# Kernel optimization log

Hardware: AMD Instinct MI355X
Metric: run time of the kernel (lower is better)

## Reference

```python
import jax, jax.numpy as jnp
import numpy as np

N_NODES = 20000
N_EDGES = 120000
IN_CH = 128
HID = 128
OUT_CH = 40
N_LAYERS = 2


def _build_two_hop(edge_index_np, num_nodes):
    # Faithful to build_two_hop_edges: for each node i, set of neighbors-of-neighbors, minus i.
    row, col = edge_index_np[0], edge_index_np[1]
    deg = np.bincount(row, minlength=num_nodes)
    order = np.argsort(row, kind='stable')
    col_sorted = col[order]
    indptr = np.zeros(num_nodes + 1, dtype=np.int64)
    indptr[1:] = np.cumsum(deg)
    reps = deg[col]                      # second-hop fanout per edge
    starts = indptr[col]
    total = int(reps.sum())
    cum = np.cumsum(reps) - reps
    offs = np.arange(total, dtype=np.int64) - np.repeat(cum, reps)
    flat = np.repeat(starts, reps) + offs
    r2 = np.repeat(row, reps)
    c2 = col_sorted[flat]
    mask = r2 != c2                      # remove i from its own 2-hop set
    keys = r2[mask].astype(np.int64) * num_nodes + c2[mask].astype(np.int64)
    uk = np.unique(keys)                 # set-dedup semantics
    return np.stack([uk // num_nodes, uk % num_nodes], axis=0)


def setup_inputs() -> dict:
    key = jax.random.key(0)
    ks = jax.random.split(key, 10)
    x = jax.random.normal(ks[0], (N_NODES, IN_CH), dtype=jnp.float32)
    x0 = jax.random.normal(ks[1], (N_NODES, IN_CH), dtype=jnp.float32)
    edge_index = jax.random.randint(ks[2], (2, N_EDGES), 0, N_NODES, dtype=jnp.int64)
    ei_np = np.asarray(edge_index)
    edge_index_2hop = jnp.asarray(_build_two_hop(ei_np, N_NODES), dtype=jnp.int64)
    s_in = 1.0 / np.sqrt(IN_CH)
    s_h = 1.0 / np.sqrt(HID)
    in_W = jax.random.normal(ks[3], (IN_CH, HID), dtype=jnp.float32) * s_in
    skip_W = jax.random.normal(ks[4], (HID, HID), dtype=jnp.float32) * s_h
    conv_W = jax.random.normal(ks[5], (N_LAYERS, HID, HID), dtype=jnp.float32) * s_h
    conv_b = jax.random.normal(ks[6], (N_LAYERS, HID), dtype=jnp.float32) * 0.01
    fc_W = jax.random.normal(ks[7], (HID, OUT_CH), dtype=jnp.float32) * s_h
    fc_b = jax.random.normal(ks[8], (OUT_CH,), dtype=jnp.float32) * 0.01
    return {"x": x, "x0": x0, "edge_index": edge_index, "edge_index_2hop": edge_index_2hop,
            "in_W": in_W, "skip_W": skip_W, "conv_W": conv_W, "conv_b": conv_b,
            "fc_W": fc_W, "fc_b": fc_b}


def _gamma(x_agg, row, col, inv_deg, n):
    # gather -> squared diff -> per-node mean -> tanh ; p=2 so abs()**2 == square
    d = x_agg[row] - x_agg[col]                 # [E, H]
    s = jnp.sum(d * d, axis=-1)                 # [E]
    g = jax.ops.segment_sum(s, row, num_segments=n) * inv_deg
    return jnp.tanh(g)[:, None]                 # [N, 1], broadcasts over H


def _forward(x, x0, edge_index, edge_index_2hop, in_W, skip_W, conv_W, conv_b, fc_W, fc_b):
    n = x.shape[0]
    row, col = edge_index[0], edge_index[1]
    row2, col2 = edge_index_2hop[0], edge_index_2hop[1]
    h = x @ in_W
    h0 = x0 @ in_W
    x_skip = h0 @ skip_W                        # same every layer (skip_fc(x0))
    ones1 = jnp.ones(row.shape[0], dtype=h.dtype)
    ones2 = jnp.ones(row2.shape[0], dtype=h.dtype)
    inv_deg1 = 1.0 / (jax.ops.segment_sum(ones1, row, num_segments=n) + 1e-10)
    inv_deg2 = 1.0 / (jax.ops.segment_sum(ones2, row2, num_segments=n) + 1e-10)
    for l in range(conv_W.shape[0]):
        # GCNConv with normalize=None(False): plain sum-aggregation of transformed source feats
        m = h @ conv_W[l]
        x_agg = jax.nn.relu(jax.ops.segment_sum(m[row], col, num_segments=n) + conv_b[l])
        g_smooth = _gamma(x_agg, row, col, inv_deg1, n)
        g_squash = _gamma(x_agg, row2, col2, inv_deg2, n)
        denom = 1.0 + g_smooth + g_squash
        h = (h + g_smooth * x_agg + g_squash * x_skip) / denom
    return h @ fc_W + fc_b


def reference(x, x0, edge_index, edge_index_2hop, in_W, skip_W, conv_W, conv_b, fc_W, fc_b):
    return _forward(x, x0, edge_index, edge_index_2hop, in_W, skip_W, conv_W, conv_b, fc_W, fc_b)
```

## Files before the change

kernel.cpp:

```cpp
#include <hip/hip_runtime.h>
#include <hip/hip_bf16.h>

#define HIDC 128
#define OUTC 40
#define ASTR 136
#define PACKN (4 * 16384 + 6144)

typedef __hip_bfloat16 bf16;
typedef unsigned int uint32;
typedef __attribute__((ext_vector_type(8))) short s8v;
typedef __attribute__((ext_vector_type(4))) float f4v;

__device__ __forceinline__ unsigned short f2b(float v) {
    return __bfloat16_as_ushort(__float2bfloat16(v));
}
__device__ __forceinline__ int ldi(const int* p, size_t i, int is64) {
    return is64 ? p[2 * i] : p[i];
}
__device__ __forceinline__ float diff2(uint32 ua, uint32 ub) {
    float ax = __uint_as_float(ua << 16);
    float ay = __uint_as_float(ua & 0xFFFF0000u);
    float bx = __uint_as_float(ub << 16);
    float by = __uint_as_float(ub & 0xFFFF0000u);
    float d0 = ax - bx, d1 = ay - by;
    return d0 * d0 + d1 * d1;
}
__device__ __forceinline__ float dq4(uint4 a, uint4 b) {
    return diff2(a.x, b.x) + diff2(a.y, b.y) + diff2(a.z, b.z) + diff2(a.w, b.w);
}

__device__ __forceinline__ void mfma16(const unsigned short* a_lds, const unsigned short* Wp,
                                       int w, int lane, f4v acc[2]) {
    const int m = lane & 15;
    const int kq = (lane >> 4) * 8;
#pragma unroll
    for (int nt2 = 0; nt2 < 2; ++nt2) {
        const int nt = w * 2 + nt2;
        f4v a = {0.f, 0.f, 0.f, 0.f};
#pragma unroll
        for (int s = 0; s < 4; ++s) {
            s8v af = *(const s8v*)(a_lds + m * ASTR + s * 32 + kq);
            s8v bfv = *(const s8v*)(Wp + (((nt * 4 + s) * 64 + lane) * 8));
            a = __builtin_amdgcn_mfma_f32_16x16x32_bf16(af, bfv, a, 0, 0, 0);
        }
        acc[nt2] = a;
    }
}

__global__ void detect_zero(const uint32* __restrict__ x, const uint32* __restrict__ e1,
                            int* __restrict__ flags, int* __restrict__ cnt2, int n2) {
    for (int i = blockIdx.x * 256 + threadIdx.x; i < n2; i += gridDim.x * 256) cnt2[i] = 0;
    if (blockIdx.x != 0) return;
    __shared__ int sh[2];
    const int t = threadIdx.x;
    if (t < 2) sh[t] = 0;
    __syncthreads();
    int cnt = 0;
    for (int i = t; i < 1024; i += 256) {
        uint32 w = x[i] & 0xFFFFu;
        uint32 e = (w >> 7) & 0xFFu;
        if ((e >= 100u && e <= 140u) || (w & 0x7FFFu) == 0u) cnt++;
    }
    int zc = (e1[2 * t + 1] == 0) ? 1 : 0;
    atomicAdd(&sh[0], cnt);
    atomicAdd(&sh[1], zc);
    __syncthreads();
    if (t == 0) {
        flags[0] = (sh[0] >= 512) ? 1 : 0;
        flags[1] = (sh[1] >= 255) ? 1 : 0;
        flags[2] = 1;
    }
}

__global__ void pack_k(const float* __restrict__ inW, const float* __restrict__ skW,
                       const float* __restrict__ cW, const float* __restrict__ fW,
                       unsigned short* __restrict__ Wp) {
    int idx = blockIdx.x * 256 + threadIdx.x;
    if (idx >= PACKN) return;
    if (idx < 4 * 16384) {
        int mat = idx >> 14, r = idx & 16383;
        const float* W = (mat == 0) ? inW
                       : (mat == 1) ? skW
                                    : cW + (size_t)(mat - 2) * HIDC * HIDC;
        int j = r & 7, lane = (r >> 3) & 63, s = (r >> 9) & 3, nt = r >> 11;
        int k = s * 32 + (lane >> 4) * 8 + j;
        int ncol = nt * 16 + (lane & 15);
        Wp[idx] = f2b(W[k * HIDC + ncol]);
    } else {
        int r = idx - 4 * 16384;
        int j = r & 7, lane = (r >> 3) & 63, s = (r >> 9) & 3, nt = r >> 11;
        int k = s * 32 + (lane >> 4) * 8 + j;
        int ncol = nt * 16 + (lane & 15);
        Wp[idx] = (ncol < OUTC) ? f2b(fW[k * OUTC + ncol]) : 0;
    }
}

__global__ void prep_k(const int* __restrict__ e2, int E2, int* __restrict__ indptr2,
                       const int* __restrict__ e1, int E1, int* __restrict__ cntC,
                       int* __restrict__ cntR, int* __restrict__ flags, int n, int L) {
    const int is64 = flags[1];
    for (int i = blockIdx.x * 256 + threadIdx.x; i < L; i += gridDim.x * 256) {
        if (i < E2 - 1 && ldi(e2, i, is64) > ldi(e2, i + 1, is64)) flags[2] = 0;
        if (i <= n) {
            int lo = 0, hi = E2;
            while (lo < hi) {
                int mid = (lo + hi) >> 1;
                if (ldi(e2, mid, is64) < i) lo = mid + 1; else hi = mid;
            }
            indptr2[i] = lo;
        }
        if (i < E1) {
            atomicAdd(&cntC[ldi(e1, (size_t)E1 + i, is64)], 1);
            atomicAdd(&cntR[ldi(e1, i, is64)], 1);
        }
    }
}

__global__ void beacon_k(const int* __restrict__ flags, float wsterm, float* __restrict__ out) {
    if (threadIdx.x == 0)
        out[0] = 100.f + 1600.f * flags[0] + 800.f * flags[1] + wsterm;
}

__global__ void scanA2(const int* __restrict__ cntC, const int* __restrict__ cntR,
                       int* __restrict__ indptrC, int* __restrict__ indptrR,
                       int* __restrict__ totals, int n, int nb) {
    __shared__ int smem[1024];
    const int half = (blockIdx.x >= nb) ? 1 : 0;
    const int b = blockIdx.x - half * nb;
    const int* cnt = half ? cntR : cntC;
    int* indptr = half ? indptrR : indptrC;
    const int tid = threadIdx.x;
    const int i = b * 1024 + tid;
    int v = (i < n) ? cnt[i] : 0;
    smem[tid] = v;
    __syncthreads();
    for (int off = 1; off < 1024; off <<= 1) {
        int tv = (tid >= off) ? smem[tid - off] : 0;
        __syncthreads();
        smem[tid] += tv;
        __syncthreads();
    }
    if (i < n) indptr[i] = smem[tid] - v;
    if (tid == 1023) totals[blockIdx.x] = smem[1023];
}

__global__ void scanB2(int* __restrict__ indptrC, int* __restrict__ indptrR,
                       int* __restrict__ curC, int* __restrict__ curR,
                       const int* __restrict__ totals, int n, int nb) {
    const int half = (blockIdx.x >= nb) ? 1 : 0;
    const int b = blockIdx.x - half * nb;
    int* indptr = half ? indptrR : indptrC;
    int* cursor = half ? curR : curC;
    const int* tot = totals + half * nb;
    const int i = b * 1024 + threadIdx.x;
    int off = 0;
    for (int k = 0; k < b; ++k) off += tot[k];
    if (i < n) {
        int fin = indptr[i] + off;
        indptr[i] = fin;
        cursor[i] = fin;
    }
    if (b == nb - 1 && threadIdx.x == 1023) indptr[n] = off + tot[b];
}

__global__ void fill_both(const int* __restrict__ e, int E, int* __restrict__ curC,
                          int* __restrict__ curR, int* __restrict__ permA,
                          int* __restrict__ permG, const int* __restrict__ flags) {
    const int is64 = flags[1];
    int i = blockIdx.x * 256 + threadIdx.x;
    if (i >= E) return;
    int r = ldi(e, i, is64);
    int c = ldi(e, (size_t)E + i, is64);
    permA[atomicAdd(&curC[c], 1)] = r;
    permG[atomicAdd(&curR[r], 1)] = c;
}

__global__ void zero_id2_fb(float* __restrict__ id2, int n, const int* __restrict__ flags) {
    if (flags[2] != 0) return;
    for (int i = blockIdx.x * 256 + threadIdx.x; i < n; i += gridDim.x * 256) id2[i] = 0.f;
}
__global__ void deg_count_fb(const int* __restrict__ e, int E, float* __restrict__ deg,
                             const int* __restrict__ flags) {
    if (flags[2] != 0) return;
    const int is64 = flags[1];
    for (int i = blockIdx.x * 256 + threadIdx.x; i < E; i += gridDim.x * 256)
        atomicAdd(&deg[ldi(e, i, is64)], 1.0f);
}
__global__ void invert_fb(float* __restrict__ d, int n, const int* __restrict__ flags) {
    if (flags[2] != 0) return;
    for (int i = blockIdx.x * 256 + threadIdx.x; i < n; i += gridDim.x * 256)
        d[i] = 1.0f / (d[i] + 1e-10f);
}
__global__ void gamma_edge_fb(const uint32* __restrict__ aggbf, const int* __restrict__ e, int E,
                              float* __restrict__ g, const int* __restrict__ flags) {
    if (flags[2] != 0) return;
    const int is64 = flags[1];
    const int lane = threadIdx.x & 63;
    const int l16 = lane & 15, sub = lane >> 4;
    const int wv0 = (blockIdx.x * 256 + threadIdx.x) >> 6;
    const int totalW = (gridDim.x * 256) >> 6;
    for (size_t base = (size_t)wv0 * 4; base < (size_t)E; base += (size_t)totalW * 4) {
        size_t ed = base + sub;
        float s = 0.f;
        int r = 0;
        bool act = ed < (size_t)E;
        if (act) {
            r = is64 ? e[2 * ed] : e[ed];
            int c = is64 ? e[2 * ((size_t)E + ed)] : e[(size_t)E + ed];
            uint4 a = ((const uint4*)(aggbf + (size_t)r * 64))[l16];
            uint4 b = ((const uint4*)(aggbf + (size_t)c * 64))[l16];
            s = dq4(a, b);
        }
#pragma unroll
        for (int off = 1; off <= 8; off <<= 1) s += __shfl_xor(s, off);
        if (l16 == 0 && act) atomicAdd(&g[r], s);
    }
}
__global__ void update_fb(float* __restrict__ h, const unsigned short* __restrict__ aggbf,
                          const float* __restrict__ xskip, const float* __restrict__ g1,
                          const float* __restrict__ g2, const int* __restrict__ indptrR,
                          const float* __restrict__ id2, unsigned short* __restrict__ hbf,
                          const int* __restrict__ flags, int n) {
    if (flags[2] != 0) return;
    for (int idx = blockIdx.x * 256 + threadIdx.x; idx < n * 32; idx += gridDim.x * 256) {
        int node = idx >> 5;
        float d1 = (float)(indptrR[node + 1] - indptrR[node]);
        float gs = tanhf(g1[node] / (d1 + 1e-10f));
        float gq = tanhf(g2[node] * id2[node]);
        float inv = 1.0f / (1.0f + gs + gq);
        float4 hv = ((const float4*)h)[idx];
        uint2 ub = ((const uint2*)aggbf)[idx];
        float4 av;
        av.x = __uint_as_float(ub.x << 16);
        av.y = __uint_as_float(ub.x & 0xFFFF0000u);
        av.z = __uint_as_float(ub.y << 16);
        av.w = __uint_as_float(ub.y & 0xFFFF0000u);
        float4 sv = ((const float4*)xskip)[idx];
        hv.x = (hv.x + gs * av.x + gq * sv.x) * inv;
        hv.y = (hv.y + gs * av.y + gq * sv.y) * inv;
        hv.z = (hv.z + gs * av.z + gq * sv.z) * inv;
        hv.w = (hv.w + gs * av.w + gq * sv.w) * inv;
        ((float4*)h)[idx] = hv;
        uint2 hb;
        hb.x = ((uint32)f2b(hv.y) << 16) | f2b(hv.x);
        hb.y = ((uint32)f2b(hv.w) << 16) | f2b(hv.z);
        ((uint2*)hbf)[idx] = hb;
    }
}

__global__ void gemm_head(const float* __restrict__ x, const float* __restrict__ x0,
                          const unsigned short* __restrict__ inWp,
                          const unsigned short* __restrict__ skWp,
                          float* __restrict__ h, unsigned short* __restrict__ hbf,
                          float* __restrict__ xskip, int n, int gB) {
    __shared__ unsigned short a_bf[16 * ASTR];
    const int pathB = (blockIdx.x >= gB) ? 1 : 0;
    const int row0 = (blockIdx.x - pathB * gB) * 16;
    const int t = threadIdx.x;
    const int lane = t & 63, w = t >> 6;
    {
        const float* A = pathB ? x0 : x;
        int i = t >> 4;
        int c0 = (t & 15) * 8;
        int r = row0 + i;
        unsigned short u[8];
        if (r < n) {
            const float* p = A + (size_t)r * HIDC + c0;
            float4 v0 = ((const float4*)p)[0];
            float4 v1 = ((const float4*)p)[1];
            u[0] = f2b(v0.x); u[1] = f2b(v0.y); u[2] = f2b(v0.z); u[3] = f2b(v0.w);
            u[4] = f2b(v1.x); u[5] = f2b(v1.y); u[6] = f2b(v1.z); u[7] = f2b(v1.w);
        } else {
#pragma unroll
            for (int j2 = 0; j2 < 8; ++j2) u[j2] = 0;
        }
        *(s8v*)(a_bf + i * ASTR + c0) = *(s8v*)u;
    }
    __syncthreads();
    f4v acc[2];
    mfma16(a_bf, inWp, w, lane, acc);
    if (!pathB) {
#pragma unroll
        for (int nt2 = 0; nt2 < 2; ++nt2) {
            int col = (w * 2 + nt2) * 16 + (lane & 15);
            int rb = row0 + (lane >> 4) * 4;
#pragma unroll
            for (int q = 0; q < 4; ++q)
                if (rb + q < n) {
                    h[(size_t)(rb + q) * HIDC + col] = acc[nt2][q];
                    hbf[(size_t)(rb + q) * HIDC + col] = f2b(acc[nt2][q]);
                }
        }
        return;
    }
    __syncthreads();
#pragma unroll
    for (int nt2 = 0; nt2 < 2; ++nt2) {
        int col = (w * 2 + nt2) * 16 + (lane & 15);
        int rb = (lane >> 4) * 4;
#pragma unroll
        for (int q = 0; q < 4; ++q)
            a_bf[(rb + q) * ASTR + col] = f2b(acc[nt2][q]);
    }
    __syncthreads();
    mfma16(a_bf, skWp, w, lane, acc);
#pragma unroll
    for (int nt2 = 0; nt2 < 2; ++nt2) {
        int col = (w * 2 + nt2) * 16 + (lane & 15);
        int rb = row0 + (lane >> 4) * 4;
#pragma unroll
        for (int q = 0; q < 4; ++q)
            if (rb + q < n) xskip[(size_t)(rb + q) * HIDC + col] = acc[nt2][q];
    }
}

__global__ void agg_gemm_relu(const unsigned short* __restrict__ hbf,
                              const int* __restrict__ indptrC,
                              const int* __restrict__ permA,
                              const unsigned short* __restrict__ cWp,
                              const float* __restrict__ cbv,
                              unsigned short* __restrict__ aggbf,
                              float* __restrict__ g2, const int* __restrict__ flags, int n) {
    if (flags[2] == 0) {
        int i = blockIdx.x * 256 + threadIdx.x;
        if (i < n) g2[i] = 0.f;
    }
    __shared__ unsigned short a_bf[16 * ASTR];
    const int row0 = blockIdx.x * 16;
    const int lane = threadIdx.x & 63, w = threadIdx.x >> 6;
    {
        const int rb = row0 + w * 4;
        float2 acc[4];
        int js[4], je[4], nxt[4];
#pragma unroll
        for (int i = 0; i < 4; ++i) {
            acc[i] = make_float2(0.f, 0.f);
            int r = rb + i;
            js[i] = (r < n) ? indptrC[r] : 0;
            je[i] = (r < n) ? indptrC[r + 1] : 0;
            nxt[i] = (js[i] < je[i]) ? permA[js[i]] : 0;
        }
        int maxd = 0;
#pragma unroll
        for (int i = 0; i < 4; ++i) maxd = max(maxd, je[i] - js[i]);
        for (int jj = 0; jj < maxd; ++jj) {
#pragma unroll
            for (int i = 0; i < 4; ++i) {
                int j = js[i] + jj;
                if (j < je[i]) {
                    int src = nxt[i];
                    int j2 = j + 1;
                    nxt[i] = (j2 < je[i]) ? permA[j2] : 0;
                    uint32 v = ((const uint32*)(hbf + (size_t)src * HIDC))[lane];
                    acc[i].x += __uint_as_float(v << 16);
                    acc[i].y += __uint_as_float(v & 0xFFFF0000u);
                }
            }
        }
#pragma unroll
        for (int i = 0; i < 4; ++i) {
            unsigned short* p = a_bf + (w * 4 + i) * ASTR + 2 * lane;
            p[0] = f2b(acc[i].x);
            p[1] = f2b(acc[i].y);
        }
    }
    __syncthreads();
    f4v acc2[2];
    mfma16(a_bf, cWp, w, lane, acc2);
#pragma unroll
    for (int nt2 = 0; nt2 < 2; ++nt2) {
        int col = (w * 2 + nt2) * 16 + (lane & 15);
        float bias = cbv[col];
        int rb = row0 + (lane >> 4) * 4;
#pragma unroll
        for (int q = 0; q < 4; ++q) {
            int r = rb + q;
            if (r < n) aggbf[(size_t)r * HIDC + col] = f2b(fmaxf(acc2[nt2][q] + bias, 0.f));
        }
    }
}

__global__ void gamma_update(const uint32* __restrict__ aggbf, const int* __restrict__ indptrR,
                             const int* __restrict__ permG, const int* __restrict__ e2, int E2,
                             const int* __restrict__ indptr2, float* __restrict__ h,
                             const float* __restrict__ xskip, float* __restrict__ g1,
                             unsigned short* __restrict__ hbf,
                             const int* __restrict__ flags, int n) {
    int r = (blockIdx.x * 256 + threadIdx.x) >> 6;
    if (r >= n) return;
    const int lane = threadIdx.x & 63;
    const int l16 = lane & 15, sub = lane >> 4;
    const int sorted = flags[2];
    const int is64 = flags[1];
    const int js1 = indptrR[r], je1 = indptrR[r + 1];
    uint4 a = ((const uint4*)(aggbf + (size_t)r * 64))[l16];
    float s1 = 0.f;
    for (int j = js1 + sub; j < je1; j += 4) {
        int c = permG[j];
        uint4 b = ((const uint4*)(aggbf + (size_t)c * 64))[l16];
        s1 += dq4(a, b);
    }
#pragma unroll
    for (int off = 32; off; off >>= 1) s1 += __shfl_xor(s1, off);
    if (sorted == 0) {
        if (lane == 0) g1[r] = s1;
        return;
    }
    const int js2 = indptr2[r], je2 = indptr2[r + 1];
    float s2a = 0.f, s2b = 0.f, s2c = 0.f, s2d = 0.f;
    int j = js2 + sub;
    for (; j + 12 < je2; j += 16) {
        int c0 = is64 ? e2[2 * ((size_t)E2 + j)] : e2[(size_t)E2 + j];
        int c1 = is64 ? e2[2 * ((size_t)E2 + j + 4)] : e2[(size_t)E2 + j + 4];
        int c2 = is64 ? e2[2 * ((size_t)E2 + j + 8)] : e2[(size_t)E2 + j + 8];
        int c3 = is64 ? e2[2 * ((size_t)E2 + j + 12)] : e2[(size_t)E2 + j + 12];
        uint4 b0 = ((const uint4*)(aggbf + (size_t)c0 * 64))[l16];
        uint4 b1 = ((const uint4*)(aggbf + (size_t)c1 * 64))[l16];
        uint4 b2 = ((const uint4*)(aggbf + (size_t)c2 * 64))[l16];
        uint4 b3 = ((const uint4*)(aggbf + (size_t)c3 * 64))[l16];
        s2a += dq4(a, b0);
        s2b += dq4(a, b1);
        s2c += dq4(a, b2);
        s2d += dq4(a, b3);
    }
    for (; j < je2; j += 4) {
        int c = is64 ? e2[2 * ((size_t)E2 + j)] : e2[(size_t)E2 + j];
        uint4 b = ((const uint4*)(aggbf + (size_t)c * 64))[l16];
        s2a += dq4(a, b);
    }
    float s2 = (s2a + s2b) + (s2c + s2d);
#pragma unroll
    for (int off = 32; off; off >>= 1) s2 += __shfl_xor(s2, off);
    float gs = tanhf(s1 / ((float)(je1 - js1) + 1e-10f));
    float gq = tanhf(s2 / ((float)(je2 - js2) + 1e-10f));
    float inv = 1.0f / (1.0f + gs + gq);
    size_t base = (size_t)r * 64 + lane;
    float2 hv = ((float2*)h)[base];
    uint32 ub = aggbf[base];
    float avx = __uint_as_float(ub << 16);
    float avy = __uint_as_float(ub & 0xFFFF0000u);
    float2 sv = ((const float2*)xskip)[base];
    hv.x = (hv.x + gs * avx + gq * sv.x) * inv;
    hv.y = (hv.y + gs * avy + gq * sv.y) * inv;
    ((float2*)h)[base] = hv;
    ((uint32*)hbf)[base] = ((uint32)f2b(hv.y) << 16) | f2b(hv.x);
}

__global__ void gemm_out(const unsigned short* __restrict__ hbf,
                         const unsigned short* __restrict__ fWp,
                         const float* __restrict__ fcb, float* __restrict__ out, int n) {
    __shared__ unsigned short a_bf[16 * ASTR];
    const int row0 = blockIdx.x * 16;
    const int t = threadIdx.x;
    const int lane = t & 63, w = t >> 6;
    {
        int i = t >> 4;
        int c0 = (t & 15) * 8;
        int r = row0 + i;
        s8v v = {0, 0, 0, 0, 0, 0, 0, 0};
        if (r < n) v = *(const s8v*)(hbf + (size_t)r * HIDC + c0);
        *(s8v*)(a_bf + i * ASTR + c0) = v;
    }
    __syncthreads();
    if (w < 3) {
        const int m = lane & 15;
        const int kq = (lane >> 4) * 8;
        f4v a = {0.f, 0.f, 0.f, 0.f};
#pragma unroll
        for (int s = 0; s < 4; ++s) {
            s8v af = *(const s8v*)(a_bf + m * ASTR + s * 32 + kq);
            s8v bfv = *(const s8v*)(fWp + (((w * 4 + s) * 64 + lane) * 8));
            a = __builtin_amdgcn_mfma_f32_16x16x32_bf16(af, bfv, a, 0, 0, 0);
        }
        int col = w * 16 + (lane & 15);
        if (col < OUTC) {
            float bias = fcb[col];
            int rb = row0 + (lane >> 4) * 4;
#pragma unroll
            for (int q = 0; q < 4; ++q)
                if (rb + q < n) out[(size_t)(rb + q) * OUTC + col] = a[q] + bias;
        }
    }
}

extern "C" void kernel_launch(void* const* d_in, const int* in_sizes, int n_in,
                              void* d_out, int out_size, void* d_ws, size_t ws_size,
                              hipStream_t stream) {
    const float* x   = (const float*)d_in[0];
    const float* x0  = (const float*)d_in[1];
    const int*   e1  = (const int*)d_in[2];
    const int*   e2  = (const int*)d_in[3];
    const float* inW = (const float*)d_in[4];
    const float* skW = (const float*)d_in[5];
    const float* cW  = (const float*)d_in[6];
    const float* cb  = (const float*)d_in[7];
    const float* fW  = (const float*)d_in[8];
    const float* fb  = (const float*)d_in[9];
    float* out = (float*)d_out;

    const int N = in_sizes[0] / HIDC;
    int div = 2;
    if (in_sizes[2] / 2 != 120000 && in_sizes[2] / 4 == 120000) div = 4;
    const int E1 = in_sizes[2] / div;
    const int E2 = in_sizes[3] / div;

    int*            flags   = (int*)d_ws;
    float*          h       = (float*)((char*)d_ws + 256);
    float*          xskip   = h + (size_t)N * HIDC;
    float*          g1      = xskip + (size_t)N * HIDC;
    float*          g2      = g1 + N;
    float*          id2     = g2 + N;
    unsigned short* aggbf   = (unsigned short*)(id2 + N);
    unsigned short* hbf     = aggbf + (size_t)N * HIDC;
    int*            indptr2 = (int*)(hbf + (size_t)N * HIDC);
    int*            cntC    = indptr2 + (N + 1);
    int*            cntR    = cntC + N;
    int*            indptrC = cntR + N;
    int*            permA   = indptrC + (N + 1);
    int*            indptrR = permA + E1;
    int*            permG   = indptrR + (N + 1);
    int*            totals  = permG + E1;
    unsigned short* Wp      = (unsigned short*)(((uintptr_t)(totals + 128) + 15) & ~(uintptr_t)15);

    const size_t FULL_REQ = 256 + ((size_t)2 * N * HIDC + 3 * N) * 4 +
                            (size_t)2 * N * HIDC * 2 +
                            ((size_t)3 * (N + 1) + 2 * N + 2 * (size_t)E1 + 128) * 4 +
                            16 + (size_t)PACKN * 2;

    detect_zero<<<(2 * N + 255) / 256, 256, 0, stream>>>(
        (const uint32*)x, (const uint32*)e1, flags, cntC, 2 * N);

    if (ws_size < FULL_REQ) {
        float wsterm = 16.f * (float)((ws_size >> 20) > 49 ? 49 : (ws_size >> 20));
        beacon_k<<<1, 64, 0, stream>>>(flags, wsterm, out);
        return;
    }

    pack_k<<<(PACKN + 255) / 256, 256, 0, stream>>>(inW, skW, cW, fW, Wp);

    int L = E2 > E1 ? E2 : E1;
    if (N + 1 > L) L = N + 1;
    prep_k<<<(L + 255) / 256, 256, 0, stream>>>(e2, E2, indptr2, e1, E1, cntC, cntR,
                                                flags, N, L);

    const int nb1024 = (N + 1023) / 1024;
    scanA2<<<2 * nb1024, 1024, 0, stream>>>(cntC, cntR, indptrC, indptrR, totals, N, nb1024);
    scanB2<<<2 * nb1024, 1024, 0, stream>>>(indptrC, indptrR, cntC, cntR, totals, N, nb1024);
    fill_both<<<(E1 + 255) / 256, 256, 0, stream>>>(e1, E1, cntC, cntR, permA, permG, flags);

    zero_id2_fb<<<64, 256, 0, stream>>>(id2, N, flags);
    deg_count_fb<<<128, 256, 0, stream>>>(e2, E2, id2, flags);
    invert_fb<<<64, 256, 0, stream>>>(id2, N, flags);

    const int gB = (N + 15) / 16;
    gemm_head<<<2 * gB, 256, 0, stream>>>(x, x0, Wp, Wp + 16384, h, hbf, xskip, N, gB);

    const int gammaBlocks = (int)(((size_t)N * 64 + 255) / 256);

    for (int l = 0; l < 2; ++l) {
        agg_gemm_relu<<<gB, 256, 0, stream>>>(
            hbf, indptrC, permA, Wp + (size_t)(2 + l) * 16384, cb + (size_t)l * HIDC,
            aggbf, g2, flags, N);
        gamma_update<<<gammaBlocks, 256, 0, stream>>>(
            (const uint32*)aggbf, indptrR, permG, e2, E2, indptr2, h, xskip, g1, hbf,
            flags, N);
        gamma_edge_fb<<<256, 256, 0, stream>>>((const uint32*)aggbf, e2, E2, g2, flags);
        update_fb<<<256, 256, 0, stream>>>(h, aggbf, xskip, g1, g2, indptrR, id2, hbf,
                                           flags, N);
    }

    gemm_out<<<gB, 256, 0, stream>>>(hbf, Wp + 4 * 16384, fb, out, N);
}
```

Baseline: 272.2 us.

## Fuse fallback kernels into gamma_update and prefetch neighbor indices

Folds the id2 zeroing into detect_zero, removes the invert kernel by dividing inside update_fb, and merges the fallback 2-hop edge kernel into gamma_update as extra blocks. It also software-prefetches permG and 2-hop column indices one iteration ahead and interleaves the s1/s2 wave reductions. The aim is fewer kernel launches and hidden index-load latency in the gather loops, at the cost of extra registers and 256 extra blocks that exit early on the sorted path.

```diff
diff --git a/kernel.cpp b/kernel.cpp
--- a/kernel.cpp
+++ b/kernel.cpp
@@ -48,8 +48,10 @@
 }
 
 __global__ void detect_zero(const uint32* __restrict__ x, const uint32* __restrict__ e1,
-                            int* __restrict__ flags, int* __restrict__ cnt2, int n2) {
+                            int* __restrict__ flags, int* __restrict__ cnt2, int n2,
+                            float* __restrict__ id2, int n) {
     for (int i = blockIdx.x * 256 + threadIdx.x; i < n2; i += gridDim.x * 256) cnt2[i] = 0;
+    for (int i = blockIdx.x * 256 + threadIdx.x; i < n; i += gridDim.x * 256) id2[i] = 0.f;
     if (blockIdx.x != 0) return;
     __shared__ int sh[2];
     const int t = threadIdx.x;
@@ -175,46 +177,12 @@
     permG[atomicAdd(&curR[r], 1)] = c;
 }
 
-__global__ void zero_id2_fb(float* __restrict__ id2, int n, const int* __restrict__ flags) {
-    if (flags[2] != 0) return;
-    for (int i = blockIdx.x * 256 + threadIdx.x; i < n; i += gridDim.x * 256) id2[i] = 0.f;
-}
 __global__ void deg_count_fb(const int* __restrict__ e, int E, float* __restrict__ deg,
                              const int* __restrict__ flags) {
     if (flags[2] != 0) return;
     const int is64 = flags[1];
     for (int i = blockIdx.x * 256 + threadIdx.x; i < E; i += gridDim.x * 256)
         atomicAdd(&deg[ldi(e, i, is64)], 1.0f);
-}
-__global__ void invert_fb(float* __restrict__ d, int n, const int* __restrict__ flags) {
-    if (flags[2] != 0) return;
-    for (int i = blockIdx.x * 256 + threadIdx.x; i < n; i += gridDim.x * 256)
-        d[i] = 1.0f / (d[i] + 1e-10f);
-}
-__global__ void gamma_edge_fb(const uint32* __restrict__ aggbf, const int* __restrict__ e, int E,
-                              float* __restrict__ g, const int* __restrict__ flags) {
-    if (flags[2] != 0) return;
-    const int is64 = flags[1];
-    const int lane = threadIdx.x & 63;
-    const int l16 = lane & 15, sub = lane >> 4;
-    const int wv0 = (blockIdx.x * 256 + threadIdx.x) >> 6;
-    const int totalW = (gridDim.x * 256) >> 6;
-    for (size_t base = (size_t)wv0 * 4; base < (size_t)E; base += (size_t)totalW * 4) {
-        size_t ed = base + sub;
-        float s = 0.f;
-        int r = 0;
-        bool act = ed < (size_t)E;
-        if (act) {
-            r = is64 ? e[2 * ed] : e[ed];
-            int c = is64 ? e[2 * ((size_t)E + ed)] : e[(size_t)E + ed];
-            uint4 a = ((const uint4*)(aggbf + (size_t)r * 64))[l16];
-            uint4 b = ((const uint4*)(aggbf + (size_t)c * 64))[l16];
-            s = dq4(a, b);
-        }
-#pragma unroll
-        for (int off = 1; off <= 8; off <<= 1) s += __shfl_xor(s, off);
-        if (l16 == 0 && act) atomicAdd(&g[r], s);
-    }
 }
 __global__ void update_fb(float* __restrict__ h, const unsigned short* __restrict__ aggbf,
                           const float* __restrict__ xskip, const float* __restrict__ g1,
@@ -226,7 +194,7 @@
         int node = idx >> 5;
         float d1 = (float)(indptrR[node + 1] - indptrR[node]);
         float gs = tanhf(g1[node] / (d1 + 1e-10f));
-        float gq = tanhf(g2[node] * id2[node]);
+        float gq = tanhf(g2[node] / (id2[node] + 1e-10f));
         float inv = 1.0f / (1.0f + gs + gq);
         float4 hv = ((const float4*)h)[idx];
         uint2 ub = ((const uint2*)aggbf)[idx];
@@ -384,40 +352,79 @@
                              const int* __restrict__ permG, const int* __restrict__ e2, int E2,
                              const int* __restrict__ indptr2, float* __restrict__ h,
                              const float* __restrict__ xskip, float* __restrict__ g1,
-                             unsigned short* __restrict__ hbf,
-                             const int* __restrict__ flags, int n) {
-    int r = (blockIdx.x * 256 + threadIdx.x) >> 6;
-    if (r >= n) return;
+                             float* __restrict__ g2fb, unsigned short* __restrict__ hbf,
+                             const int* __restrict__ flags, int n, int nodeBlocks) {
     const int lane = threadIdx.x & 63;
     const int l16 = lane & 15, sub = lane >> 4;
     const int sorted = flags[2];
     const int is64 = flags[1];
+    if (blockIdx.x >= nodeBlocks) {
+        if (sorted != 0) return;
+        const int b2 = blockIdx.x - nodeBlocks;
+        const int wv0 = (b2 * 256 + threadIdx.x) >> 6;
+        const int totalW = (256 * 256) >> 6;
+        for (size_t base = (size_t)wv0 * 4; base < (size_t)E2; base += (size_t)totalW * 4) {
+            size_t ed = base + sub;
+            float s = 0.f;
+            int r = 0;
+            bool act = ed < (size_t)E2;
+            if (act) {
+                r = is64 ? e2[2 * ed] : e2[ed];
+                int c = is64 ? e2[2 * ((size_t)E2 + ed)] : e2[(size_t)E2 + ed];
+                uint4 a = ((const uint4*)(aggbf + (size_t)r * 64))[l16];
+                uint4 b = ((const uint4*)(aggbf + (size_t)c * 64))[l16];
+                s = dq4(a, b);
+            }
+#pragma unroll
+            for (int off = 1; off <= 8; off <<= 1) s += __shfl_xor(s, off);
+            if (l16 == 0 && act) atomicAdd(&g2fb[r], s);
+        }
+        return;
+    }
+    int r = (blockIdx.x * 256 + threadIdx.x) >> 6;
+    if (r >= n) return;
     const int js1 = indptrR[r], je1 = indptrR[r + 1];
+    const int js2 = indptr2[r], je2 = indptr2[r + 1];
     uint4 a = ((const uint4*)(aggbf + (size_t)r * 64))[l16];
+    int j = js2 + sub;
+    int c0 = 0, c1 = 0, c2 = 0, c3 = 0;
+    if (j + 12 < je2) {
+        c0 = is64 ? e2[2 * ((size_t)E2 + j)] : e2[(size_t)E2 + j];
+        c1 = is64 ? e2[2 * ((size_t)E2 + j + 4)] : e2[(size_t)E2 + j + 4];
+        c2 = is64 ? e2[2 * ((size_t)E2 + j + 8)] : e2[(size_t)E2 + j + 8];
+        c3 = is64 ? e2[2 * ((size_t)E2 + j + 12)] : e2[(size_t)E2 + j + 12];
+    }
     float s1 = 0.f;
-    for (int j = js1 + sub; j < je1; j += 4) {
-        int c = permG[j];
-        uint4 b = ((const uint4*)(aggbf + (size_t)c * 64))[l16];
-        s1 += dq4(a, b);
-    }
-#pragma unroll
-    for (int off = 32; off; off >>= 1) s1 += __shfl_xor(s1, off);
+    {
+        int j1 = js1 + sub;
+        int cn = (j1 < je1) ? permG[j1] : 0;
+        for (; j1 < je1; j1 += 4) {
+            int c = cn;
+            int jn = j1 + 4;
+            cn = (jn < je1) ? permG[jn] : 0;
+            uint4 b = ((const uint4*)(aggbf + (size_t)c * 64))[l16];
+            s1 += dq4(a, b);
+        }
+    }
     if (sorted == 0) {
+#pragma unroll
+        for (int off = 32; off; off >>= 1) s1 += __shfl_xor(s1, off);
         if (lane == 0) g1[r] = s1;
         return;
     }
-    const int js2 = indptr2[r], je2 = indptr2[r + 1];
     float s2a = 0.f, s2b = 0.f, s2c = 0.f, s2d = 0.f;
-    int j = js2 + sub;
     for (; j + 12 < je2; j += 16) {
-        int c0 = is64 ? e2[2 * ((size_t)E2 + j)] : e2[(size_t)E2 + j];
-        int c1 = is64 ? e2[2 * ((size_t)E2 + j + 4)] : e2[(size_t)E2 + j + 4];
-        int c2 = is64 ? e2[2 * ((size_t)E2 + j + 8)] : e2[(size_t)E2 + j + 8];
-        int c3 = is64 ? e2[2 * ((size_t)E2 + j + 12)] : e2[(size_t)E2 + j + 12];
         uint4 b0 = ((const uint4*)(aggbf + (size_t)c0 * 64))[l16];
         uint4 b1 = ((const uint4*)(aggbf + (size_t)c1 * 64))[l16];
         uint4 b2 = ((const uint4*)(aggbf + (size_t)c2 * 64))[l16];
         uint4 b3 = ((const uint4*)(aggbf + (size_t)c3 * 64))[l16];
+        int jn = j + 16;
+        if (jn + 12 < je2) {
+            c0 = is64 ? e2[2 * ((size_t)E2 + jn)] : e2[(size_t)E2 + jn];
+            c1 = is64 ? e2[2 * ((size_t)E2 + jn + 4)] : e2[(size_t)E2 + jn + 4];
+            c2 = is64 ? e2[2 * ((size_t)E2 + jn + 8)] : e2[(size_t)E2 + jn + 8];
+            c3 = is64 ? e2[2 * ((size_t)E2 + jn + 12)] : e2[(size_t)E2 + jn + 12];
+        }
         s2a += dq4(a, b0);
         s2b += dq4(a, b1);
         s2c += dq4(a, b2);
@@ -430,7 +437,10 @@
     }
     float s2 = (s2a + s2b) + (s2c + s2d);
 #pragma unroll
-    for (int off = 32; off; off >>= 1) s2 += __shfl_xor(s2, off);
+    for (int off = 32; off; off >>= 1) {
+        s1 += __shfl_xor(s1, off);
+        s2 += __shfl_xor(s2, off);
+    }
     float gs = tanhf(s1 / ((float)(je1 - js1) + 1e-10f));
     float gq = tanhf(s2 / ((float)(je2 - js2) + 1e-10f));
     float inv = 1.0f / (1.0f + gs + gq);
@@ -528,7 +538,7 @@
                             16 + (size_t)PACKN * 2;
 
     detect_zero<<<(2 * N + 255) / 256, 256, 0, stream>>>(
-        (const uint32*)x, (const uint32*)e1, flags, cntC, 2 * N);
+        (const uint32*)x, (const uint32*)e1, flags, cntC, 2 * N, id2, N);
 
     if (ws_size < FULL_REQ) {
         float wsterm = 16.f * (float)((ws_size >> 20) > 49 ? 49 : (ws_size >> 20));
@@ -548,9 +558,7 @@
     scanB2<<<2 * nb1024, 1024, 0, stream>>>(indptrC, indptrR, cntC, cntR, totals, N, nb1024);
     fill_both<<<(E1 + 255) / 256, 256, 0, stream>>>(e1, E1, cntC, cntR, permA, permG, flags);
 
-    zero_id2_fb<<<64, 256, 0, stream>>>(id2, N, flags);
     deg_count_fb<<<128, 256, 0, stream>>>(e2, E2, id2, flags);
-    invert_fb<<<64, 256, 0, stream>>>(id2, N, flags);
 
     const int gB = (N + 15) / 16;
     gemm_head<<<2 * gB, 256, 0, stream>>>(x, x0, Wp, Wp + 16384, h, hbf, xskip, N, gB);
@@ -561,10 +569,9 @@
         agg_gemm_relu<<<gB, 256, 0, stream>>>(
             hbf, indptrC, permA, Wp + (size_t)(2 + l) * 16384, cb + (size_t)l * HIDC,
             aggbf, g2, flags, N);
-        gamma_update<<<gammaBlocks, 256, 0, stream>>>(
-            (const uint32*)aggbf, indptrR, permG, e2, E2, indptr2, h, xskip, g1, hbf,
-            flags, N);
-        gamma_edge_fb<<<256, 256, 0, stream>>>((const uint32*)aggbf, e2, E2, g2, flags);
+        gamma_update<<<gammaBlocks + 256, 256, 0, stream>>>(
+            (const uint32*)aggbf, indptrR, permG, e2, E2, indptr2, h, xskip, g1, g2, hbf,
+            flags, N, gammaBlocks);
         update_fb<<<256, 256, 0, stream>>>(h, aggbf, xskip, g1, g2, indptrR, id2, hbf,
                                            flags, N);
     }
```

Measured after the change: 251.2 us. 1.08x faster.
